# Optimization experiments

Measured on AMD Instinct MI355X. Metric: run time of the kernel, lower is better.

## Reference

```python
import jax, jax.numpy as jnp
import numpy as np

N_HEADS = 16
N_KV_HEADS = 4
HEAD_DIM = 64
ROPE_BASE = 10000.0

def _rope_cos_sin(T, dtype):
    # flash-attn style: cos/sin of shape [T, head_dim//2]
    inv_freq = 1.0 / (ROPE_BASE ** (jnp.arange(0, HEAD_DIM, 2, dtype=jnp.float32) / HEAD_DIM))
    freqs = jnp.arange(T, dtype=jnp.float32)[:, None] * inv_freq[None, :]  # [T, D/2]
    return jnp.cos(freqs).astype(dtype), jnp.sin(freqs).astype(dtype)

def _apply_rope(x, cos, sin):
    # x: [B, H, T, D], non-interleaved rotate-half on full head dim
    d2 = HEAD_DIM // 2
    x1, x2 = x[..., :d2], x[..., d2:]
    c = cos[None, None, :, :]
    s = sin[None, None, :, :]
    return jnp.concatenate([x1 * c - x2 * s, x2 * c + x1 * s], axis=-1)

def setup_inputs() -> dict:
    key = jax.random.key(0)
    ks = jax.random.split(key, 6)
    B, T, D = 1, 4096, 1024
    def g(k, shape, scale):
        return jax.random.normal(k, shape, dtype=jnp.float32) * scale
    return {
        "query": g(ks[0], (B, T, D), 1.0),
        "Wq": g(ks[1], (D, D), D ** -0.5),
        "Wk": g(ks[2], (D, N_KV_HEADS * HEAD_DIM), D ** -0.5),
        "Wv": g(ks[3], (D, N_KV_HEADS * HEAD_DIM), D ** -0.5),
        "W1": g(ks[4], (D, 4 * D), D ** -0.5),
        "W2": g(ks[5], (4 * D, D), (4 * D) ** -0.5),
    }

def reference(query, Wq, Wk, Wv, W1, W2):
    B, T, D = query.shape
    # QKV projections -> [B, H, T, Dh]
    q = (query @ Wq).reshape(B, T, N_HEADS, HEAD_DIM).transpose(0, 2, 1, 3)
    k = (query @ Wk).reshape(B, T, N_KV_HEADS, HEAD_DIM).transpose(0, 2, 1, 3)
    v = (query @ Wv).reshape(B, T, N_KV_HEADS, HEAD_DIM).transpose(0, 2, 1, 3)
    # RoPE (seqlen_offset = 0, no cache)
    cos, sin = _rope_cos_sin(T, q.dtype)
    q = _apply_rope(q, cos, sin)
    k = _apply_rope(k, cos, sin)
    # GQA: repeat KV heads to match Q heads
    n_rep = N_HEADS // N_KV_HEADS
    k = jnp.repeat(k, n_rep, axis=1)
    v = jnp.repeat(v, n_rep, axis=1)
    # Scaled dot-product attention, causal
    scale = HEAD_DIM ** -0.5
    scores = jnp.einsum("bhqd,bhkd->bhqk", q, k) * scale
    i = jnp.arange(T)[:, None]
    j = jnp.arange(T)[None, :]
    scores = jnp.where(j > i, jnp.finfo(scores.dtype).min, scores)
    attn = jax.nn.softmax(scores, axis=-1)
    out = jnp.einsum("bhqk,bhkd->bhqd", attn, v)  # [B, H, T, Dh]
    out = out.transpose(0, 2, 1, 3).reshape(B, T, D)
    # out_proj: Linear -> SiLU -> Linear (use_swiglu=True path)
    return jax.nn.silu(out @ W1) @ W2
```

## Files before the change

### kernel.cpp

```cpp
#include <hip/hip_runtime.h>
#include <stdint.h>

typedef unsigned short u16;
typedef __bf16 bf16x8 __attribute__((ext_vector_type(8)));
typedef float f32x4 __attribute__((ext_vector_type(4)));

#define T_SEQ 4096
#define DMODEL 1024

__device__ __forceinline__ float bf2f(u16 x) {
  union { uint32_t u; float f; } v; v.u = ((uint32_t)x) << 16; return v.f;
}
__device__ __forceinline__ u16 f2bf(float f) {
  union { float f; uint32_t u; } v; v.f = f;
  return (u16)((v.u + 0x7FFFu + ((v.u >> 16) & 1u)) >> 16);
}
__device__ __forceinline__ float fexp2(float x) {
#if __has_builtin(__builtin_amdgcn_exp2f)
  return __builtin_amdgcn_exp2f(x);
#else
  return __expf(x * 0.6931471805599453f);
#endif
}
__device__ __forceinline__ uint32_t pack_bf16(float lo, float hi) {
#if __has_builtin(__builtin_amdgcn_cvt_pk_bf16_f32)
  typedef __bf16 bf16x2_t __attribute__((ext_vector_type(2)));
  union { bf16x2_t v; uint32_t u; } c;
  c.v = __builtin_amdgcn_cvt_pk_bf16_f32(lo, hi);
  return c.u;
#else
  union { float f; uint32_t u; } a, b;
  a.f = lo; b.f = hi;
  return __builtin_amdgcn_perm(b.u + 0x8000u, a.u + 0x8000u, 0x07060302u);
#endif
}
__device__ __forceinline__ void async16(void* lds, const void* g) {
  __builtin_amdgcn_global_load_lds(
      (__attribute__((address_space(1))) void*)const_cast<void*>(g),
      (__attribute__((address_space(3))) void*)lds, 16, 0, 0);
}
__device__ __forceinline__ void storeC(u16* C, size_t i, float v) { C[i] = f2bf(v); }
__device__ __forceinline__ void storeC(float* C, size_t i, float v) { C[i] = v; }

__device__ __forceinline__ void wtrans_body(const float* __restrict__ in,
                                            u16* __restrict__ out, int K, int N,
                                            int bx, int by, int tid,
                                            float (*tile)[65]) {
  const int n0 = bx * 64, k0 = by * 64;
  const int r = tid >> 2, c = (tid & 3) * 16;
#pragma unroll
  for (int j = 0; j < 4; ++j) {
    float4 v = *(const float4*)&in[(size_t)(k0 + r) * N + n0 + c + j * 4];
    tile[r][c + j * 4 + 0] = v.x; tile[r][c + j * 4 + 1] = v.y;
    tile[r][c + j * 4 + 2] = v.z; tile[r][c + j * 4 + 3] = v.w;
  }
  __syncthreads();
  union { u16 s[16]; uint4 q[2]; } buf;
#pragma unroll
  for (int j = 0; j < 16; ++j) buf.s[j] = f2bf(tile[c + j][r]);
  u16* dst = out + (size_t)(n0 + r) * K + k0 + c;
  *(uint4*)(dst) = buf.q[0];
  *(uint4*)(dst + 8) = buf.q[1];
}

__global__ void __launch_bounds__(256) prep(const float* __restrict__ query,
                                            const float* __restrict__ Wq,
                                            const float* __restrict__ Wk,
                                            const float* __restrict__ Wv,
                                            const float* __restrict__ W1,
                                            const float* __restrict__ W2,
                                            u16* __restrict__ Xb,
                                            u16* __restrict__ WqkvT,
                                            u16* __restrict__ W1T,
                                            u16* __restrict__ W2T) {
  __shared__ float tile[64][65];
  const int b = blockIdx.x, tid = threadIdx.x;
  if (b < 4096) {
    int idx = (b * 256 + tid) * 4;
    float4 v = *(const float4*)(query + idx);
    union { u16 s[4]; uint2 q; } o;
    o.s[0] = f2bf(v.x); o.s[1] = f2bf(v.y); o.s[2] = f2bf(v.z); o.s[3] = f2bf(v.w);
    *(uint2*)(Xb + idx) = o.q;
  } else if (b < 4352) {
    int t = b - 4096;
    wtrans_body(Wq, WqkvT, 1024, 1024, t & 15, t >> 4, tid, tile);
  } else if (b < 4416) {
    int t = b - 4352;
    wtrans_body(Wk, WqkvT + (size_t)1024 * 1024, 1024, 256, t & 3, t >> 2, tid, tile);
  } else if (b < 4480) {
    int t = b - 4416;
    wtrans_body(Wv, WqkvT + (size_t)1280 * 1024, 1024, 256, t & 3, t >> 2, tid, tile);
  } else if (b < 5504) {
    int t = b - 4480;
    wtrans_body(W1, W1T, 1024, 4096, t & 63, t >> 6, tid, tile);
  } else {
    int t = b - 5504;
    wtrans_body(W2, W2T, 4096, 1024, t & 15, t >> 4, tid, tile);
  }
}

__global__ void __launch_bounds__(256) rope_vt(const u16* __restrict__ qkv,
                                               u16* __restrict__ Q,
                                               u16* __restrict__ Ko,
                                               u16* __restrict__ Vt) {
  __shared__ u16 tile[64][65];
  const int b = blockIdx.x, tid = threadIdx.x;
  if (b < 4096) {
    const int t = b;
    const int i = tid & 31;
    const float ang = (float)t * powf(10000.f, -(float)i * (1.f / 32.f));
    float s, c;
    sincosf(ang, &s, &c);
    const u16* row = qkv + (size_t)t * 1536;
    const float QS = 0.125f * 1.4426950408889634f;
    const float cq = c * QS, sq = s * QS;
#pragma unroll
    for (int it = 0; it < 2; ++it) {
      int h = (tid >> 5) + it * 8;
      float x1 = bf2f(row[h * 64 + i]);
      float x2 = bf2f(row[h * 64 + 32 + i]);
      size_t o = ((size_t)h * T_SEQ + t) * 64 + i;
      Q[o] = f2bf(x1 * cq - x2 * sq);
      Q[o + 32] = f2bf(x2 * cq + x1 * sq);
    }
    if (tid < 128) {
      int h = tid >> 5;
      float x1 = bf2f(row[1024 + h * 64 + i]);
      float x2 = bf2f(row[1024 + h * 64 + 32 + i]);
      size_t o = ((size_t)h * T_SEQ + t) * 64 + i;
      Ko[o] = f2bf(x1 * c - x2 * s);
      Ko[o + 32] = f2bf(x2 * c + x1 * s);
    }
  } else {
    const int t = b - 4096;
    const int t0 = (t & 63) * 64, h = t >> 6;
    const int r = tid >> 2, q4 = (tid & 3) * 16;
    const u16* src = qkv + (size_t)(t0 + r) * 1536 + 1280 + h * 64 + q4;
    union { u16 s[16]; uint4 q[2]; } buf;
    buf.q[0] = *(const uint4*)(src);
    buf.q[1] = *(const uint4*)(src + 8);
#pragma unroll
    for (int j = 0; j < 16; ++j) tile[r][q4 + j] = buf.s[j];
    __syncthreads();
#pragma unroll
    for (int j = 0; j < 16; ++j) buf.s[j] = tile[q4 + j][r];
    u16* dst = Vt + ((size_t)h * 64 + r) * T_SEQ + t0 + q4;
    *(uint4*)(dst) = buf.q[0];
    *(uint4*)(dst + 8) = buf.q[1];
  }
}

template <int AM, int ACT, typename OutT>
__global__ void __launch_bounds__(256) gemm_bt(const u16* __restrict__ A,
                                               const u16* __restrict__ Bt,
                                               OutT* __restrict__ C,
                                               int M, int N, int K) {
  __shared__ u16 sA[AM * 32][64];
  __shared__ u16 sB[128][64];
  const int tid = threadIdx.x;
  const int w = tid >> 6, lane = tid & 63;
  const int g = lane >> 4, l15 = lane & 15;
  const int r8 = lane >> 3, c8 = lane & 7;
  const int bm = blockIdx.y * (AM * 32), bn = blockIdx.x * 128;

  f32x4 acc[AM][4];
#pragma unroll
  for (int i = 0; i < AM; ++i)
#pragma unroll
    for (int j = 0; j < 4; ++j) acc[i][j] = (f32x4){0.f, 0.f, 0.f, 0.f};

  const u16* Ag = A + (size_t)(bm + w * (AM * 8) + r8) * K + (c8 ^ r8) * 8;
  const u16* Bg = Bt + (size_t)(bn + w * 32 + r8) * K + (c8 ^ r8) * 8;
  const int mrow = (w >> 1) * (AM * 16), ncol = (w & 1) * 64;
  const int swz = l15 & 7;

  for (int k0 = 0; k0 < K; k0 += 64) {
#pragma unroll
    for (int t = 0; t < AM; ++t)
      async16(&sA[w * (AM * 8) + t * 8][0], Ag + (size_t)(t * 8) * K + k0);
#pragma unroll
    for (int t = 0; t < 4; ++t)
      async16(&sB[w * 32 + t * 8][0], Bg + (size_t)(t * 8) * K + k0);
    __syncthreads();
#pragma unroll
    for (int kk = 0; kk < 2; ++kk) {
      const int cb = ((kk * 4 + g) ^ swz) * 8;
      bf16x8 a[AM], b[4];
#pragma unroll
      for (int i = 0; i < AM; ++i) a[i] = *(const bf16x8*)&sA[mrow + i * 16 + l15][cb];
#pragma unroll
      for (int i = 0; i < 4; ++i) b[i] = *(const bf16x8*)&sB[ncol + i * 16 + l15][cb];
#pragma unroll
      for (int mi = 0; mi < AM; ++mi)
#pragma unroll
        for (int ni = 0; ni < 4; ++ni)
          acc[mi][ni] = __builtin_amdgcn_mfma_f32_16x16x32_bf16(a[mi], b[ni], acc[mi][ni], 0, 0, 0);
    }
    __syncthreads();
  }
#pragma unroll
  for (int mi = 0; mi < AM; ++mi)
#pragma unroll
    for (int ni = 0; ni < 4; ++ni)
#pragma unroll
      for (int r = 0; r < 4; ++r) {
        int row = bm + mrow + mi * 16 + g * 4 + r;
        int col = bn + ncol + ni * 16 + l15;
        float v = acc[mi][ni][r];
        if (ACT == 1) v = v / (1.f + __expf(-v));
        storeC(C, (size_t)row * N + col, v);
      }
}

__global__ void __launch_bounds__(256, 2) gemm_w2(const u16* __restrict__ A,
                                                  const u16* __restrict__ Bt,
                                                  float* __restrict__ C0,
                                                  u16* __restrict__ C1) {
  __shared__ u16 sA[128][64];
  __shared__ u16 sB[128][64];
  const int K = 4096, N = 1024;
  const int z = blockIdx.z, koff = z * 2048;
  const int tid = threadIdx.x;
  const int w = tid >> 6, lane = tid & 63;
  const int g = lane >> 4, l15 = lane & 15;
  const int r8 = lane >> 3, c8 = lane & 7;
  const int bm = blockIdx.y * 128, bn = blockIdx.x * 128;

  f32x4 acc[4][4];
#pragma unroll
  for (int i = 0; i < 4; ++i)
#pragma unroll
    for (int j = 0; j < 4; ++j) acc[i][j] = (f32x4){0.f, 0.f, 0.f, 0.f};

  const u16* Ag = A + (size_t)(bm + w * 32 + r8) * K + koff + (c8 ^ r8) * 8;
  const u16* Bg = Bt + (size_t)(bn + w * 32 + r8) * K + koff + (c8 ^ r8) * 8;
  const int mrow = (w >> 1) * 64, ncol = (w & 1) * 64;
  const int swz = l15 & 7;

  for (int k0 = 0; k0 < 2048; k0 += 64) {
#pragma unroll
    for (int t = 0; t < 4; ++t) {
      async16(&sA[w * 32 + t * 8][0], Ag + (size_t)(t * 8) * K + k0);
      async16(&sB[w * 32 + t * 8][0], Bg + (size_t)(t * 8) * K + k0);
    }
    __syncthreads();
#pragma unroll
    for (int kk = 0; kk < 2; ++kk) {
      const int cb = ((kk * 4 + g) ^ swz) * 8;
      bf16x8 a[4], b[4];
#pragma unroll
      for (int i = 0; i < 4; ++i) {
        a[i] = *(const bf16x8*)&sA[mrow + i * 16 + l15][cb];
        b[i] = *(const bf16x8*)&sB[ncol + i * 16 + l15][cb];
      }
#pragma unroll
      for (int mi = 0; mi < 4; ++mi)
#pragma unroll
        for (int ni = 0; ni < 4; ++ni)
          acc[mi][ni] = __builtin_amdgcn_mfma_f32_16x16x32_bf16(a[mi], b[ni], acc[mi][ni], 0, 0, 0);
    }
    __syncthreads();
  }
#pragma unroll
  for (int mi = 0; mi < 4; ++mi)
#pragma unroll
    for (int ni = 0; ni < 4; ++ni)
#pragma unroll
      for (int r = 0; r < 4; ++r) {
        size_t idx = (size_t)(bm + mrow + mi * 16 + g * 4 + r) * N + bn + ncol + ni * 16 + l15;
        if (z == 0) C0[idx] = acc[mi][ni][r];
        else        C1[idx] = f2bf(acc[mi][ni][r]);
      }
}

__global__ void __launch_bounds__(256) w2_combine(float* __restrict__ out,
                                                  const u16* __restrict__ P1) {
  int idx = (blockIdx.x * 256 + threadIdx.x) * 4;
  float4 v = *(const float4*)(out + idx);
  union { uint2 q; u16 s[4]; } p;
  p.q = *(const uint2*)(P1 + idx);
  v.x += bf2f(p.s[0]); v.y += bf2f(p.s[1]);
  v.z += bf2f(p.s[2]); v.w += bf2f(p.s[3]);
  *(float4*)(out + idx) = v;
}

__global__ void __launch_bounds__(256, 2) attn(const u16* __restrict__ Q,
                                               const u16* __restrict__ K,
                                               const u16* __restrict__ Vt,
                                               u16* __restrict__ O0,
                                               u16* __restrict__ O1,
                                               float* __restrict__ L0,
                                               float* __restrict__ L1) {
  __shared__ u16 sK[2][64][64];
  __shared__ u16 sV[2][64][64];
  __shared__ u16 sP[4][64][68];
  const int pr = blockIdx.x >> 1;
  const int split = blockIdx.x & 1;
  const int h = blockIdx.y;
  const int kvh = h >> 2;
  const int tid = threadIdx.x;
  const int w = tid >> 6, lane = tid & 63;
  const int g = lane >> 4, l15 = lane & 15;
  const int r8 = lane >> 3, c8 = lane & 7;
  const int swz = l15 & 7;
  const int t0 = pr, t1 = 31 - pr;
  const int off = split * 64;

  u16* Op = split ? O1 : O0;
  float* Lp = split ? L1 : L0;

  bf16x8 qf[2][2][2];
  {
    const u16* Qh = Q + (size_t)h * T_SEQ * 64;
#pragma unroll
    for (int half = 0; half < 2; ++half)
#pragma unroll
      for (int mi = 0; mi < 2; ++mi) {
        const int q = (half ? t1 : t0) * 128 + w * 32 + mi * 16 + l15;
#pragma unroll
        for (int kk = 0; kk < 2; ++kk)
          qf[half][mi][kk] = *(const bf16x8*)(Qh + (size_t)q * 64 + (kk * 4 + g) * 8);
      }
  }

  f32x4 oacc[2][2][4];
  f32x4 lacc[2][2];
#pragma unroll
  for (int half = 0; half < 2; ++half)
#pragma unroll
    for (int mi = 0; mi < 2; ++mi) {
      lacc[half][mi] = (f32x4){0.f, 0.f, 0.f, 0.f};
#pragma unroll
      for (int nd = 0; nd < 4; ++nd) oacc[half][mi][nd] = (f32x4){0.f, 0.f, 0.f, 0.f};
    }

  bf16x8 ONES;
  {
    union { u16 s[8]; bf16x8 v; } o;
#pragma unroll
    for (int i = 0; i < 8; ++i) o.s[i] = 0x3F80;
    ONES = o.v;
  }

  const u16* Kg = K + ((size_t)kvh * T_SEQ + w * 16 + r8) * 64 + (c8 ^ r8) * 8;
  const u16* Vg = Vt + ((size_t)kvh * 64 + w * 16 + r8) * T_SEQ + (c8 ^ r8) * 8;

#define STAGE(J, B)                                                     \
  {                                                                     \
    const int kv0_ = (J) * 64;                                          \
    async16(&sK[B][w * 16 + 0][0], Kg + (size_t)kv0_ * 64);             \
    async16(&sK[B][w * 16 + 8][0], Kg + (size_t)(kv0_ + 8) * 64);       \
    async16(&sV[B][w * 16 + 0][0], Vg + kv0_);                          \
    async16(&sV[B][w * 16 + 8][0], Vg + (size_t)8 * T_SEQ + kv0_);      \
  }

#define BODY(B, ACT0, M0, M1)                                                     \
  {                                                                               \
    const int b_ = (B);                                                           \
    f32x4 s1[2][4], s0[2][4];                                                     \
    _Pragma("unroll") for (int mi = 0; mi < 2; ++mi)                              \
    _Pragma("unroll") for (int kt = 0; kt < 4; ++kt) {                            \
      s1[mi][kt] = (f32x4){0.f, 0.f, 0.f, 0.f};                                   \
      if (ACT0) s0[mi][kt] = (f32x4){0.f, 0.f, 0.f, 0.f};                         \
    }                                                                             \
    _Pragma("unroll") for (int kt = 0; kt < 4; ++kt)                              \
    _Pragma("unroll") for (int kk = 0; kk < 2; ++kk) {                            \
      bf16x8 kf = *(const bf16x8*)&sK[b_][kt * 16 + l15][((kk * 4 + g) ^ swz) * 8]; \
      _Pragma("unroll") for (int mi = 0; mi < 2; ++mi) {                          \
        s1[mi][kt] = __builtin_amdgcn_mfma_f32_16x16x32_bf16(kf, qf[1][mi][kk], s1[mi][kt], 0, 0, 0); \
        if (ACT0)                                                                 \
          s0[mi][kt] = __builtin_amdgcn_mfma_f32_16x16x32_bf16(kf, qf[0][mi][kk], s0[mi][kt], 0, 0, 0); \
      }                                                                           \
    }                                                                             \
    _Pragma("unroll") for (int mi = 0; mi < 2; ++mi) {                            \
      const int thr_ = w * 32 + mi * 16 + l15 - off;                              \
      _Pragma("unroll") for (int kt = 0; kt < 4; ++kt) {                          \
        float p_[4];                                                              \
        _Pragma("unroll") for (int r = 0; r < 4; ++r) {                           \
          float p = fexp2(s1[mi][kt][r]);                                         \
          if (M1 && (kt * 16 + g * 4 + r > thr_)) p = 0.f;                        \
          p_[r] = p;                                                              \
        }                                                                         \
        uint2 pk;                                                                 \
        pk.x = pack_bf16(p_[0], p_[1]);                                           \
        pk.y = pack_bf16(p_[2], p_[3]);                                           \
        *(uint2*)&sP[w][32 + mi * 16 + l15][kt * 16 + g * 4] = pk;                \
      }                                                                           \
      if (ACT0) {                                                                 \
        _Pragma("unroll") for (int kt = 0; kt < 4; ++kt) {                        \
          float p_[4];                                                            \
          _Pragma("unroll") for (int r = 0; r < 4; ++r) {                         \
            float p = fexp2(s0[mi][kt][r]);                                       \
            if (M0 && (kt * 16 + g * 4 + r > thr_)) p = 0.f;                      \
            p_[r] = p;                                                            \
          }                                                                       \
          uint2 pk;                                                               \
          pk.x = pack_bf16(p_[0], p_[1]);                                         \
          pk.y = pack_bf16(p_[2], p_[3]);                                         \
          *(uint2*)&sP[w][mi * 16 + l15][kt * 16 + g * 4] = pk;                   \
        }                                                                         \
      }                                                                           \
    }                                                                             \
    __builtin_amdgcn_wave_barrier();          \
    _Pragma("unroll") for (int kk = 0; kk < 2; ++kk) {                            \
      bf16x8 pf1[2], pf0[2];                                                      \
      _Pragma("unroll") for (int mi = 0; mi < 2; ++mi) {                          \
        pf1[mi] = *(const bf16x8*)&sP[w][32 + mi * 16 + l15][kk * 32 + g * 8];    \
        if (ACT0) pf0[mi] = *(const bf16x8*)&sP[w][mi * 16 + l15][kk * 32 + g * 8]; \
      }                                                                           \
      _Pragma("unroll") for (int mi = 0; mi < 2; ++mi) {                          \
        lacc[1][mi] = __builtin_amdgcn_mfma_f32_16x16x32_bf16(pf1[mi], ONES, lacc[1][mi], 0, 0, 0); \
        if (ACT0)                                                                 \
          lacc[0][mi] = __builtin_amdgcn_mfma_f32_16x16x32_bf16(pf0[mi], ONES, lacc[0][mi], 0, 0, 0); \
      }                                                                           \
      _Pragma("unroll") for (int nd = 0; nd < 4; ++nd) {                          \
        bf16x8 vf = *(const bf16x8*)&sV[b_][nd * 16 + l15][((kk * 4 + g) ^ swz) * 8]; \
        _Pragma("unroll") for (int mi = 0; mi < 2; ++mi) {                        \
          oacc[1][mi][nd] = __builtin_amdgcn_mfma_f32_16x16x32_bf16(pf1[mi], vf, oacc[1][mi][nd], 0, 0, 0); \
          if (ACT0)                                                               \
            oacc[0][mi][nd] = __builtin_amdgcn_mfma_f32_16x16x32_bf16(pf0[mi], vf, oacc[0][mi][nd], 0, 0, 0); \
        }                                                                         \
      }                                                                           \
    }                                                                             \
  }

  const int e0 = 2 * t0 + split, e1 = 2 * t1 + split;
  STAGE(split, 0);
  int jj = split, b = 0;
  for (; jj < e0; jj += 2, b ^= 1) {
    __syncthreads();
    STAGE(jj + 2, b ^ 1);
    BODY(b, true, false, false);
  }
  {
    __syncthreads();
    STAGE(jj + 2, b ^ 1);
    BODY(b, true, true, false);
    jj += 2; b ^= 1;
  }
  for (; jj < e1; jj += 2, b ^= 1) {
    __syncthreads();
    STAGE(jj + 2, b ^ 1);
    BODY(b, false, false, false);
  }
  {
    __syncthreads();
    BODY(b, false, false, true);
  }
#undef STAGE
#undef BODY

#pragma unroll
  for (int half = 0; half < 2; ++half) {
    const int tb = (half ? t1 : t0) * 128;
#pragma unroll
    for (int mi = 0; mi < 2; ++mi)
#pragma unroll
      for (int r = 0; r < 4; ++r) {
        const int trow = tb + w * 32 + mi * 16 + g * 4 + r;
#pragma unroll
        for (int nd = 0; nd < 4; ++nd)
          Op[(size_t)trow * DMODEL + h * 64 + nd * 16 + l15] = f2bf(oacc[half][mi][nd][r]);
        if (l15 == 0) Lp[h * T_SEQ + trow] = lacc[half][mi][r];
      }
  }
}

__global__ void __launch_bounds__(256) attn_combine(const u16* __restrict__ O0,
                                                    const u16* __restrict__ O1,
                                                    const float* __restrict__ L0,
                                                    const float* __restrict__ L1,
                                                    u16* __restrict__ AO) {
  const int t = blockIdx.x, tid = threadIdx.x;
  const int h = tid >> 4, d4 = (tid & 15) * 4;
  const float inv = 1.f / (L0[h * T_SEQ + t] + L1[h * T_SEQ + t]);
  const size_t idx = (size_t)t * DMODEL + h * 64 + d4;
  union { uint2 q; u16 s[4]; } a, b, o;
  a.q = *(const uint2*)(O0 + idx);
  b.q = *(const uint2*)(O1 + idx);
#pragma unroll
  for (int i = 0; i < 4; ++i) o.s[i] = f2bf((bf2f(a.s[i]) + bf2f(b.s[i])) * inv);
  *(uint2*)(AO + idx) = o.q;
}

extern "C" void kernel_launch(void* const* d_in, const int* in_sizes, int n_in,
                              void* d_out, int out_size, void* d_ws, size_t ws_size,
                              hipStream_t stream) {
  const float* query = (const float*)d_in[0];
  const float* Wq = (const float*)d_in[1];
  const float* Wk = (const float*)d_in[2];
  const float* Wv = (const float*)d_in[3];
  const float* W1 = (const float*)d_in[4];
  const float* W2 = (const float*)d_in[5];
  float* out = (float*)d_out;

  char* ws = (char*)d_ws;
  size_t off = 0;
  auto alloc = [&](size_t bytes) { char* p = ws + off; off += (bytes + 255) & ~(size_t)255; return p; };
  u16* Xb   = (u16*)alloc((size_t)4096 * 1024 * 2);
  u16* QKVb = (u16*)alloc((size_t)4096 * 1536 * 2);
  u16* Qb   = (u16*)alloc((size_t)16 * 4096 * 64 * 2);
  u16* Kb   = (u16*)alloc((size_t)4 * 4096 * 64 * 2);
  u16* Vtb  = (u16*)alloc((size_t)4 * 4096 * 64 * 2);
  u16* H    = (u16*)ws;
  u16*   O0p = Xb;
  u16*   O1p = QKVb;
  float* L0p = (float*)(QKVb + (size_t)4096 * 1024);
  float* L1p = L0p + 16 * T_SEQ;
  u16* WqkvT = (u16*)alloc((size_t)1536 * 1024 * 2);
  u16* W1T   = (u16*)alloc((size_t)4096 * 1024 * 2);
  u16* W2T   = (u16*)alloc((size_t)1024 * 4096 * 2);
  u16* AO    = (u16*)alloc((size_t)4096 * 1024 * 2);
  u16* P1    = W1T;
  (void)ws_size; (void)in_sizes; (void)n_in; (void)out_size;

  prep<<<6528, 256, 0, stream>>>(query, Wq, Wk, Wv, W1, W2, Xb, WqkvT, W1T, W2T);
  gemm_bt<2, 0, u16><<<dim3(12, 64), 256, 0, stream>>>(Xb, WqkvT, QKVb, 4096, 1536, 1024);
  rope_vt<<<4352, 256, 0, stream>>>(QKVb, Qb, Kb, Vtb);
  attn<<<dim3(32, 16), 256, 0, stream>>>(Qb, Kb, Vtb, O0p, O1p, L0p, L1p);
  attn_combine<<<4096, 256, 0, stream>>>(O0p, O1p, L0p, L1p, AO);
  gemm_bt<4, 1, u16><<<dim3(32, 32), 256, 0, stream>>>(AO, W1T, H, 4096, 4096, 1024);
  gemm_w2<<<dim3(8, 32, 2), 256, 0, stream>>>(H, W2T, out, P1);
  w2_combine<<<4096, 256, 0, stream>>>(out, P1);
}
```

Before: 283.5 us.

## Split causal attention KV range three ways and serialize the P buffer halves

The attention kernel's KV split grows from two to three per query-tile pair. Each block now strides over KV tiles by three, and diagonal masking is chosen by the tile's parity. The P staging buffer in shared memory is halved: the two query halves' probabilities are packed in registers and written and consumed one after the other, which lets launch bounds allow three blocks per SM. The goal is more blocks and better load balance across CUs. The cost is a third partial output and row sum that the combine kernel must read and add, and extra intra-wave barriers.

```diff
diff --git a/kernel.cpp b/kernel.cpp
--- a/kernel.cpp
+++ b/kernel.cpp
@@ -284,18 +284,20 @@
   *(float4*)(out + idx) = v;
 }
 
-__global__ void __launch_bounds__(256, 2) attn(const u16* __restrict__ Q,
+__global__ void __launch_bounds__(256, 3) attn(const u16* __restrict__ Q,
                                                const u16* __restrict__ K,
                                                const u16* __restrict__ Vt,
                                                u16* __restrict__ O0,
                                                u16* __restrict__ O1,
+                                               u16* __restrict__ O2,
                                                float* __restrict__ L0,
-                                               float* __restrict__ L1) {
+                                               float* __restrict__ L1,
+                                               float* __restrict__ L2) {
   __shared__ u16 sK[2][64][64];
   __shared__ u16 sV[2][64][64];
-  __shared__ u16 sP[4][64][68];
-  const int pr = blockIdx.x >> 1;
-  const int split = blockIdx.x & 1;
+  __shared__ u16 sP[4][32][68];
+  const int pr = blockIdx.x / 3;
+  const int split = blockIdx.x % 3;
   const int h = blockIdx.y;
   const int kvh = h >> 2;
   const int tid = threadIdx.x;
@@ -304,10 +306,9 @@
   const int r8 = lane >> 3, c8 = lane & 7;
   const int swz = l15 & 7;
   const int t0 = pr, t1 = 31 - pr;
-  const int off = split * 64;
-
-  u16* Op = split ? O1 : O0;
-  float* Lp = split ? L1 : L0;
+
+  u16* Op = split == 0 ? O0 : (split == 1 ? O1 : O2);
+  float* Lp = split == 0 ? L0 : (split == 1 ? L1 : L2);
 
   bf16x8 qf[2][2][2];
   {
@@ -354,7 +355,7 @@
     async16(&sV[B][w * 16 + 8][0], Vg + (size_t)8 * T_SEQ + kv0_);      \
   }
 
-#define BODY(B, ACT0, M0, M1)                                                     \
+#define BODY(B, ACT0, M0, M1, OFF)                                                \
   {                                                                               \
     const int b_ = (B);                                                           \
     f32x4 s1[2][4], s0[2][4];                                                     \
@@ -372,8 +373,9 @@
           s0[mi][kt] = __builtin_amdgcn_mfma_f32_16x16x32_bf16(kf, qf[0][mi][kk], s0[mi][kt], 0, 0, 0); \
       }                                                                           \
     }                                                                             \
+    uint2 pk1[2][4], pk0[2][4];                                                   \
     _Pragma("unroll") for (int mi = 0; mi < 2; ++mi) {                            \
-      const int thr_ = w * 32 + mi * 16 + l15 - off;                              \
+      const int thr_ = w * 32 + mi * 16 + l15 - (OFF);                            \
       _Pragma("unroll") for (int kt = 0; kt < 4; ++kt) {                          \
         float p_[4];                                                              \
         _Pragma("unroll") for (int r = 0; r < 4; ++r) {                           \
@@ -381,71 +383,78 @@
           if (M1 && (kt * 16 + g * 4 + r > thr_)) p = 0.f;                        \
           p_[r] = p;                                                              \
         }                                                                         \
-        uint2 pk;                                                                 \
-        pk.x = pack_bf16(p_[0], p_[1]);                                           \
-        pk.y = pack_bf16(p_[2], p_[3]);                                           \
-        *(uint2*)&sP[w][32 + mi * 16 + l15][kt * 16 + g * 4] = pk;                \
-      }                                                                           \
-      if (ACT0) {                                                                 \
-        _Pragma("unroll") for (int kt = 0; kt < 4; ++kt) {                        \
-          float p_[4];                                                            \
+        pk1[mi][kt].x = pack_bf16(p_[0], p_[1]);                                  \
+        pk1[mi][kt].y = pack_bf16(p_[2], p_[3]);                                  \
+        if (ACT0) {                                                               \
+          float q_[4];                                                            \
           _Pragma("unroll") for (int r = 0; r < 4; ++r) {                         \
             float p = fexp2(s0[mi][kt][r]);                                       \
             if (M0 && (kt * 16 + g * 4 + r > thr_)) p = 0.f;                      \
-            p_[r] = p;                                                            \
+            q_[r] = p;                                                            \
           }                                                                       \
-          uint2 pk;                                                               \
-          pk.x = pack_bf16(p_[0], p_[1]);                                         \
-          pk.y = pack_bf16(p_[2], p_[3]);                                         \
-          *(uint2*)&sP[w][mi * 16 + l15][kt * 16 + g * 4] = pk;                   \
+          pk0[mi][kt].x = pack_bf16(q_[0], q_[1]);                                \
+          pk0[mi][kt].y = pack_bf16(q_[2], q_[3]);                                \
         }                                                                         \
       }                                                                           \
+      _Pragma("unroll") for (int kt = 0; kt < 4; ++kt)                            \
+        *(uint2*)&sP[w][mi * 16 + l15][kt * 16 + g * 4] = pk1[mi][kt];            \
     }                                                                             \
-    __builtin_amdgcn_wave_barrier();          \
+    __builtin_amdgcn_wave_barrier();                                              \
     _Pragma("unroll") for (int kk = 0; kk < 2; ++kk) {                            \
-      bf16x8 pf1[2], pf0[2];                                                      \
-      _Pragma("unroll") for (int mi = 0; mi < 2; ++mi) {                          \
-        pf1[mi] = *(const bf16x8*)&sP[w][32 + mi * 16 + l15][kk * 32 + g * 8];    \
-        if (ACT0) pf0[mi] = *(const bf16x8*)&sP[w][mi * 16 + l15][kk * 32 + g * 8]; \
-      }                                                                           \
-      _Pragma("unroll") for (int mi = 0; mi < 2; ++mi) {                          \
+      bf16x8 pf1[2];                                                              \
+      _Pragma("unroll") for (int mi = 0; mi < 2; ++mi)                            \
+        pf1[mi] = *(const bf16x8*)&sP[w][mi * 16 + l15][kk * 32 + g * 8];         \
+      _Pragma("unroll") for (int mi = 0; mi < 2; ++mi)                            \
         lacc[1][mi] = __builtin_amdgcn_mfma_f32_16x16x32_bf16(pf1[mi], ONES, lacc[1][mi], 0, 0, 0); \
-        if (ACT0)                                                                 \
-          lacc[0][mi] = __builtin_amdgcn_mfma_f32_16x16x32_bf16(pf0[mi], ONES, lacc[0][mi], 0, 0, 0); \
-      }                                                                           \
       _Pragma("unroll") for (int nd = 0; nd < 4; ++nd) {                          \
         bf16x8 vf = *(const bf16x8*)&sV[b_][nd * 16 + l15][((kk * 4 + g) ^ swz) * 8]; \
-        _Pragma("unroll") for (int mi = 0; mi < 2; ++mi) {                        \
+        _Pragma("unroll") for (int mi = 0; mi < 2; ++mi)                          \
           oacc[1][mi][nd] = __builtin_amdgcn_mfma_f32_16x16x32_bf16(pf1[mi], vf, oacc[1][mi][nd], 0, 0, 0); \
-          if (ACT0)                                                               \
+      }                                                                           \
+    }                                                                             \
+    if (ACT0) {                                                                   \
+      __builtin_amdgcn_wave_barrier();                                            \
+      _Pragma("unroll") for (int mi = 0; mi < 2; ++mi)                            \
+      _Pragma("unroll") for (int kt = 0; kt < 4; ++kt)                            \
+        *(uint2*)&sP[w][mi * 16 + l15][kt * 16 + g * 4] = pk0[mi][kt];            \
+      __builtin_amdgcn_wave_barrier();                                            \
+      _Pragma("unroll") for (int kk = 0; kk < 2; ++kk) {                          \
+        bf16x8 pf0[2];                                                            \
+        _Pragma("unroll") for (int mi = 0; mi < 2; ++mi)                          \
+          pf0[mi] = *(const bf16x8*)&sP[w][mi * 16 + l15][kk * 32 + g * 8];       \
+        _Pragma("unroll") for (int mi = 0; mi < 2; ++mi)                          \
+          lacc[0][mi] = __builtin_amdgcn_mfma_f32_16x16x32_bf16(pf0[mi], ONES, lacc[0][mi], 0, 0, 0); \
+        _Pragma("unroll") for (int nd = 0; nd < 4; ++nd) {                        \
+          bf16x8 vf = *(const bf16x8*)&sV[b_][nd * 16 + l15][((kk * 4 + g) ^ swz) * 8]; \
+          _Pragma("unroll") for (int mi = 0; mi < 2; ++mi)                        \
             oacc[0][mi][nd] = __builtin_amdgcn_mfma_f32_16x16x32_bf16(pf0[mi], vf, oacc[0][mi][nd], 0, 0, 0); \
         }                                                                         \
       }                                                                           \
     }                                                                             \
   }
 
-  const int e0 = 2 * t0 + split, e1 = 2 * t1 + split;
+  const int tt0 = 2 * t0, tt1 = 2 * t1;
   STAGE(split, 0);
   int jj = split, b = 0;
-  for (; jj < e0; jj += 2, b ^= 1) {
-    __syncthreads();
-    STAGE(jj + 2, b ^ 1);
-    BODY(b, true, false, false);
-  }
-  {
-    __syncthreads();
-    STAGE(jj + 2, b ^ 1);
-    BODY(b, true, true, false);
-    jj += 2; b ^= 1;
-  }
-  for (; jj < e1; jj += 2, b ^= 1) {
-    __syncthreads();
-    STAGE(jj + 2, b ^ 1);
-    BODY(b, false, false, false);
-  }
-  {
-    __syncthreads();
-    BODY(b, false, false, true);
+  for (; jj < tt0; jj += 3, b ^= 1) {
+    __syncthreads();
+    STAGE(jj + 3, b ^ 1);
+    BODY(b, true, false, false, 0);
+  }
+  if (jj <= tt0 + 1) {
+    __syncthreads();
+    if (jj + 3 <= tt1 + 1) STAGE(jj + 3, b ^ 1);
+    BODY(b, true, true, false, (jj & 1) * 64);
+    jj += 3; b ^= 1;
+  }
+  for (; jj < tt1; jj += 3, b ^= 1) {
+    __syncthreads();
+    if (jj + 3 <= tt1 + 1) STAGE(jj + 3, b ^ 1);
+    BODY(b, false, false, false, 0);
+  }
+  if (jj <= tt1 + 1) {
+    __syncthreads();
+    BODY(b, false, false, true, (jj & 1) * 64);
   }
 #undef STAGE
 #undef BODY
@@ -468,18 +477,22 @@
 
 __global__ void __launch_bounds__(256) attn_combine(const u16* __restrict__ O0,
                                                     const u16* __restrict__ O1,
+                                                    const u16* O2,
                                                     const float* __restrict__ L0,
                                                     const float* __restrict__ L1,
-                                                    u16* __restrict__ AO) {
+                                                    const float* __restrict__ L2,
+                                                    u16* AO) {
   const int t = blockIdx.x, tid = threadIdx.x;
   const int h = tid >> 4, d4 = (tid & 15) * 4;
-  const float inv = 1.f / (L0[h * T_SEQ + t] + L1[h * T_SEQ + t]);
+  const float inv = 1.f / (L0[h * T_SEQ + t] + L1[h * T_SEQ + t] + L2[h * T_SEQ + t]);
   const size_t idx = (size_t)t * DMODEL + h * 64 + d4;
-  union { uint2 q; u16 s[4]; } a, b, o;
+  union { uint2 q; u16 s[4]; } a, b, c, o;
   a.q = *(const uint2*)(O0 + idx);
   b.q = *(const uint2*)(O1 + idx);
-#pragma unroll
-  for (int i = 0; i < 4; ++i) o.s[i] = f2bf((bf2f(a.s[i]) + bf2f(b.s[i])) * inv);
+  c.q = *(const uint2*)(O2 + idx);
+#pragma unroll
+  for (int i = 0; i < 4; ++i)
+    o.s[i] = f2bf((bf2f(a.s[i]) + bf2f(b.s[i]) + bf2f(c.s[i])) * inv);
   *(uint2*)(AO + idx) = o.q;
 }
 
@@ -507,18 +520,20 @@
   u16*   O1p = QKVb;
   float* L0p = (float*)(QKVb + (size_t)4096 * 1024);
   float* L1p = L0p + 16 * T_SEQ;
+  float* L2p = L1p + 16 * T_SEQ;
   u16* WqkvT = (u16*)alloc((size_t)1536 * 1024 * 2);
   u16* W1T   = (u16*)alloc((size_t)4096 * 1024 * 2);
   u16* W2T   = (u16*)alloc((size_t)1024 * 4096 * 2);
   u16* AO    = (u16*)alloc((size_t)4096 * 1024 * 2);
   u16* P1    = W1T;
+  u16* O2p   = AO;
   (void)ws_size; (void)in_sizes; (void)n_in; (void)out_size;
 
   prep<<<6528, 256, 0, stream>>>(query, Wq, Wk, Wv, W1, W2, Xb, WqkvT, W1T, W2T);
   gemm_bt<2, 0, u16><<<dim3(12, 64), 256, 0, stream>>>(Xb, WqkvT, QKVb, 4096, 1536, 1024);
   rope_vt<<<4352, 256, 0, stream>>>(QKVb, Qb, Kb, Vtb);
-  attn<<<dim3(32, 16), 256, 0, stream>>>(Qb, Kb, Vtb, O0p, O1p, L0p, L1p);
-  attn_combine<<<4096, 256, 0, stream>>>(O0p, O1p, L0p, L1p, AO);
+  attn<<<dim3(48, 16), 256, 0, stream>>>(Qb, Kb, Vtb, O0p, O1p, O2p, L0p, L1p, L2p);
+  attn_combine<<<4096, 256, 0, stream>>>(O0p, O1p, O2p, L0p, L1p, L2p, AO);
   gemm_bt<4, 1, u16><<<dim3(32, 32), 256, 0, stream>>>(AO, W1T, H, 4096, 4096, 1024);
   gemm_w2<<<dim3(8, 32, 2), 256, 0, stream>>>(H, W2T, out, P1);
   w2_combine<<<4096, 256, 0, stream>>>(out, P1);
```

Result: slower. 317.8 us (+12.1%).
